# Optimization experiments

Hardware: AMD Instinct MI355X
Metric: run time of the kernel (lower is better)

Reference implementation:

```python
import jax, jax.numpy as jnp
import numpy as np
import math

T, B, D, H, DH, DI, V, L = 1024, 4, 512, 8, 64, 2048, 256, 8
STAGES = (2, 4, 2)   # pre, shortened, post layer counts (model_config)
SF = 4               # fixed boundary every SF tokens
S = T // SF          # number of segments


def setup_inputs() -> dict:
    key = jax.random.key(0)
    ks = jax.random.split(key, 12)
    sd = 0.02
    data = jax.random.randint(ks[0], (T, B), 0, V, dtype=jnp.int32)
    t = jnp.arange(T)
    boundaries_gt = jnp.tile(((t % SF) == (SF - 1)).astype(jnp.int32)[:, None], (1, B))
    return {
        'data': data,
        'boundaries_gt': boundaries_gt,
        'word_emb': jax.random.normal(ks[1], (V, D)) * sd,
        'r_w_bias': jax.random.normal(ks[2], (H, DH)) * sd,
        'r_r_bias': jax.random.normal(ks[3], (H, DH)) * sd,
        'null_group': jax.random.normal(ks[4], (1, 1, D)),
        'down_ln_g': jnp.ones((D,), jnp.float32),
        'down_ln_b': jnp.zeros((D,), jnp.float32),
        'qkv_w': jax.random.normal(ks[5], (L, 3 * H * DH, D)) * sd,
        'rk_w': jax.random.normal(ks[6], (L, H * DH, D)) * sd,
        'o_w': jax.random.normal(ks[7], (L, D, H * DH)) * sd,
        'ln1_g': jnp.ones((L, D), jnp.float32),
        'ln1_b': jnp.zeros((L, D), jnp.float32),
        'ff_w1': jax.random.normal(ks[8], (L, DI, D)) * sd,
        'ff_b1': jnp.zeros((L, DI), jnp.float32),
        'ff_w2': jax.random.normal(ks[9], (L, D, DI)) * sd,
        'ff_b2': jnp.zeros((L, D), jnp.float32),
        'ln2_g': jnp.ones((L, D), jnp.float32),
        'ln2_b': jnp.zeros((L, D), jnp.float32),
        'final_w': jax.random.normal(ks[10], (V, D)) * sd,
        'final_b': jnp.zeros((V,), jnp.float32),
    }


def _ln(x, g, b):
    m = jnp.mean(x, -1, keepdims=True)
    v = jnp.mean((x - m) ** 2, -1, keepdims=True)
    return (x - m) * jax.lax.rsqrt(v + 1e-5) * g + b


def _pos_emb(qlen):
    # sinusoidal relative positions qlen-1 .. 0
    pos = jnp.arange(qlen - 1, -1, -1.0, dtype=jnp.float32)
    inv = 1.0 / (10000.0 ** (jnp.arange(0, D, 2, dtype=jnp.float32) / D))
    ang = pos[:, None] * inv[None, :]
    return jnp.concatenate([jnp.sin(ang), jnp.cos(ang)], -1)  # (qlen, D)


def _rel_shift(x):
    # x: (q, k, b, n) -- Transformer-XL relative shift
    q, k, b, n = x.shape
    x = jnp.pad(x, ((0, 0), (1, 0), (0, 0), (0, 0)))
    return x.reshape(k + 1, q, b, n)[1:].reshape(q, k, b, n)


def _stage(x, P, lo, hi, r_w_bias, r_r_bias):
    qkv_w, rk_w, o_w, ln1_g, ln1_b, w1, b1, w2, b2, ln2_g, ln2_b = P
    qlen, bsz, _ = x.shape
    r = _pos_emb(qlen)
    mask = jnp.triu(jnp.ones((qlen, qlen), bool), 1)  # causal
    scale = 1.0 / math.sqrt(DH)
    for i in range(lo, hi):
        h = x @ qkv_w[i].T                                  # (q,b,3HDh)
        qh, kh, vh = jnp.split(h, 3, axis=-1)
        qh = qh.reshape(qlen, bsz, H, DH)
        kh = kh.reshape(qlen, bsz, H, DH)
        vh = vh.reshape(qlen, bsz, H, DH)
        rk = (r @ rk_w[i].T).reshape(qlen, H, DH)
        AC = jnp.einsum('ibnd,jbnd->ijbn', qh + r_w_bias, kh)
        BD = _rel_shift(jnp.einsum('ibnd,jnd->ijbn', qh + r_r_bias, rk))
        score = jnp.where(mask[:, :, None, None], -1e30, (AC + BD) * scale)
        prob = jax.nn.softmax(score, axis=1)
        vec = jnp.einsum('ijbn,jbnd->ibnd', prob, vh).reshape(qlen, bsz, H * DH)
        x = _ln(x + vec @ o_w[i].T, ln1_g[i], ln1_b[i])      # post-LN
        ff = jax.nn.relu(x @ w1[i].T + b1[i]) @ w2[i].T + b2[i]
        x = _ln(x + ff, ln2_g[i], ln2_b[i])
    return x


def _downsample(bnd, hidden, null_group):
    # bnd: (B,T) float, hidden: (T,B,D). Mean-pool each segment, prepend null group.
    seg = jnp.cumsum(bnd, axis=1) - bnd                      # segment id per token
    ind = (seg[:, :, None] == jnp.arange(S, dtype=bnd.dtype)).astype(hidden.dtype)
    w = ind / (ind.sum(axis=1, keepdims=True) + 1e-9)        # (B,T,S)
    short = jnp.einsum('tbd,bts->sbd', hidden, w)
    null = jnp.tile(null_group, (1, hidden.shape[1], 1))
    return jnp.concatenate([null, short], axis=0)            # (S+1,B,D)


def _upsample(bnd, short):
    # token t copies segment cumsum(bnd)[t] (0 == null group)
    seg = jnp.cumsum(bnd, axis=1).astype(jnp.int32)          # (B,T) in [0,S]
    up = jnp.take_along_axis(short, seg.T[:, :, None], axis=0)  # (T,B,D)
    return up / (1.0 + 1e-9)                                 # matches 1/(1+eps) normalizer


def _forward(data, boundaries_gt, word_emb, r_w_bias, r_r_bias, null_group,
             down_ln_g, down_ln_b, qkv_w, rk_w, o_w, ln1_g, ln1_b,
             ff_w1, ff_b1, ff_w2, ff_b2, ln2_g, ln2_b, final_w, final_b):
    P = (qkv_w, rk_w, o_w, ln1_g, ln1_b, ff_w1, ff_b1, ff_w2, ff_b2, ln2_g, ln2_b)
    hidden = word_emb[data]                                  # (T,B,D)
    hidden = _stage(hidden, P, 0, STAGES[0], r_w_bias, r_r_bias)
    residual = hidden
    hard = boundaries_gt.astype(jnp.float32).T               # (B,T)
    short = _downsample(hard, hidden, null_group)
    short = _ln(short, down_ln_g, down_ln_b)
    short = _stage(short, P, STAGES[0], STAGES[0] + STAGES[1], r_w_bias, r_r_bias)
    hidden = _upsample(hard, short) + residual
    hidden = _stage(hidden, P, STAGES[0] + STAGES[1], L, r_w_bias, r_r_bias)
    return hidden @ final_w.T + final_b                      # logits (T,B,V)


def reference(data, boundaries_gt, word_emb, r_w_bias, r_r_bias, null_group,
              down_ln_g, down_ln_b, qkv_w, rk_w, o_w, ln1_g, ln1_b,
              ff_w1, ff_b1, ff_w2, ff_b2, ln2_g, ln2_b, final_w, final_b):
    return _forward(data, boundaries_gt, word_emb, r_w_bias, r_r_bias, null_group,
                    down_ln_g, down_ln_b, qkv_w, rk_w, o_w, ln1_g, ln1_b,
                    ff_w1, ff_b1, ff_w2, ff_b2, ln2_g, ln2_b, final_w, final_b)
```

## Files before the change

### kernel.cpp

```cpp
#include <hip/hip_runtime.h>
#include <math.h>

#define T_  1024
#define B_  4
#define D_  512
#define H_  8
#define DH_ 64
#define DI_ 2048
#define V_  256
#define L_  8
#define S_  256

typedef _Float16 f16;
typedef f16   f16x8 __attribute__((ext_vector_type(8)));
typedef float f32x4 __attribute__((ext_vector_type(4)));

__device__ __forceinline__ void gload16(const void* g, void* l) {
    __builtin_amdgcn_global_load_lds(
        (const __attribute__((address_space(1))) void*)g,
        (__attribute__((address_space(3))) void*)l, 16, 0, 0);
}

__constant__ int cIT[24] = {15,15,14,13,12,11,10, 9,  8, 7,14, 6,13, 5,12, 4,  8, 0, 9, 1,10, 2,11, 3};
__constant__ int cT0[24] = { 0, 8, 0, 0, 0, 0, 0, 0,  0, 0, 8, 0, 8, 0, 8, 0,  8, 0, 8, 0, 8, 0, 8, 0};
__constant__ int cT1[24] = { 8,16, 8, 8, 8, 8, 8, 8,  8, 8,15, 7,14, 6,13, 5,  9, 1,10, 2,11, 3,12, 4};
__constant__ int cIT2[8] = {4,4,3,3,2,2,1,0};
__constant__ int cT02[8] = {0,3,0,2,0,2,0,0};
__constant__ int cT12[8] = {3,5,2,4,2,3,2,1};

__global__ __launch_bounds__(256) void k_f2h(const float* __restrict__ s,
                                             f16* __restrict__ d, int n) {
    int i = (blockIdx.x * 256 + threadIdx.x) * 4;
    int stride = gridDim.x * 1024;
    for (; i < n; i += stride) {
        float4 v = *(const float4*)(s + i);
        d[i + 0] = (f16)v.x; d[i + 1] = (f16)v.y;
        d[i + 2] = (f16)v.z; d[i + 3] = (f16)v.w;
    }
}

__global__ __launch_bounds__(256) void k_embed(const int* __restrict__ data,
                                               const float* __restrict__ emb,
                                               float* __restrict__ x,
                                               f16* __restrict__ xh) {
    int idx = blockIdx.x * 256 + threadIdx.x;
    if (idx >= T_ * B_ * D_) return;
    int d  = idx & (D_ - 1);
    int tb = idx >> 9;
    float v = emb[(size_t)data[tb] * D_ + d];
    x[idx] = v; xh[idx] = (f16)v;
}

__global__ __launch_bounds__(256) void k_posemb(f16* __restrict__ r, int qlen) {
    int p = blockIdx.x;
    int k = threadIdx.x;
    float pos = (float)(qlen - 1 - p);
    float inv = powf(10000.f, -((float)k) / 256.f);
    float ang = pos * inv;
    r[(size_t)p * D_ + k]       = (f16)sinf(ang);
    r[(size_t)p * D_ + 256 + k] = (f16)cosf(ang);
}

template<int BM, int BN, int OUT16, int ACT>
__global__ __launch_bounds__(256) void k_gemm(const f16* __restrict__ X, int lda,
                                              const f16* __restrict__ W,
                                              const float* __restrict__ bias,
                                              void* __restrict__ Yv,
                                              int M, int N, int K) {
    __shared__ f16 As[BM * 64];
    __shared__ f16 Bs[BN * 64];
    const int tid = threadIdx.x, w = tid >> 6, lane = tid & 63;
    const int l16 = lane & 15, lg = lane >> 4;
    int nwg = gridDim.x * gridDim.y;
    int bid = blockIdx.y * gridDim.x + blockIdx.x;
    if ((nwg & 7) == 0) bid = (bid & 7) * (nwg >> 3) + (bid >> 3);
    const int bm = (bid % gridDim.x) * BM, bn = (bid / gridDim.x) * BN;
    const int lrow = lane >> 3, lcol = (lane & 7) * 8;
    constexpr int AI = (BM >= 32) ? BM / 32 : 1;
    constexpr int BI = BN / 32;
    constexpr int MI = (BN == 128) ? 4 : BM / 32;
    constexpr int NJ = 2;
    const int rbase = (BN == 128) ? 0 : (w >> 1) * (BM / 2);
    const int cbase = (BN == 128) ? w * 32 : (w & 1) * 32;
    const f32x4 z4 = {0.f, 0.f, 0.f, 0.f};
    f32x4 acc[MI][NJ];
    #pragma unroll
    for (int i = 0; i < MI; ++i)
        #pragma unroll
        for (int j = 0; j < NJ; ++j) acc[i][j] = z4;

    for (int k0 = 0; k0 < K; k0 += 64) {
        __syncthreads();
        #pragma unroll
        for (int u = 0; u < AI; ++u) {
            int rb = w * (BM / 4) + u * 8;
            gload16(X + (size_t)(bm + rb + lrow) * lda + k0 + lcol, &As[rb * 64]);
        }
        #pragma unroll
        for (int u = 0; u < BI; ++u) {
            int rb = w * (BN / 4) + u * 8;
            gload16(W + (size_t)(bn + rb + lrow) * K + k0 + lcol, &Bs[rb * 64]);
        }
        __syncthreads();
        __builtin_amdgcn_s_setprio(1);
        #pragma unroll
        for (int h = 0; h < 2; ++h) {
            f16x8 af[MI], bf[NJ];
            #pragma unroll
            for (int i = 0; i < MI; ++i)
                af[i] = *(const f16x8*)&As[(rbase + i * 16 + l16) * 64 + h * 32 + lg * 8];
            #pragma unroll
            for (int j = 0; j < NJ; ++j)
                bf[j] = *(const f16x8*)&Bs[(cbase + j * 16 + l16) * 64 + h * 32 + lg * 8];
            #pragma unroll
            for (int i = 0; i < MI; ++i)
                #pragma unroll
                for (int j = 0; j < NJ; ++j)
                    acc[i][j] = __builtin_amdgcn_mfma_f32_16x16x32_f16(af[i], bf[j], acc[i][j], 0, 0, 0);
        }
        __builtin_amdgcn_s_setprio(0);
    }
    #pragma unroll
    for (int i = 0; i < MI; ++i) {
        #pragma unroll
        for (int r = 0; r < 4; ++r) {
            int row = bm + rbase + i * 16 + lg * 4 + r;
            if (row >= M) continue;
            int colb = bn + cbase + l16;
            #pragma unroll
            for (int j = 0; j < NJ; ++j) {
                float v = acc[i][j][r];
                if (bias) v += bias[colb + j * 16];
                if (ACT) v = fmaxf(v, 0.f);
                if (OUT16) ((f16*)Yv)[(size_t)row * N + colb + j * 16] = (f16)v;
                else       ((float*)Yv)[(size_t)row * N + colb + j * 16] = v;
            }
        }
    }
}

__global__ __launch_bounds__(256) void k_ln(float* __restrict__ x,
                                            const f16* __restrict__ add,
                                            const float* __restrict__ g,
                                            const float* __restrict__ b,
                                            f16* __restrict__ xh, int rows) {
    int row = blockIdx.x * 4 + (threadIdx.x >> 6);
    if (row >= rows) return;
    int lane = threadIdx.x & 63;
    float* xr = x + (size_t)row * D_ + lane * 8;
    float v[8];
    {
        float4 a0 = *(const float4*)xr;
        float4 a1 = *(const float4*)(xr + 4);
        v[0] = a0.x; v[1] = a0.y; v[2] = a0.z; v[3] = a0.w;
        v[4] = a1.x; v[5] = a1.y; v[6] = a1.z; v[7] = a1.w;
    }
    if (add) {
        f16x8 a = *(const f16x8*)(add + (size_t)row * D_ + lane * 8);
        #pragma unroll
        for (int u = 0; u < 8; ++u) v[u] += (float)a[u];
    }
    float s = 0.f, sq = 0.f;
    #pragma unroll
    for (int u = 0; u < 8; ++u) { s += v[u]; sq += v[u] * v[u]; }
    #pragma unroll
    for (int off = 1; off < 64; off <<= 1) {
        s  += __shfl_xor(s,  off, 64);
        sq += __shfl_xor(sq, off, 64);
    }
    float mean = s * (1.f / (float)D_);
    float var  = sq * (1.f / (float)D_) - mean * mean;
    float rs   = rsqrtf(var + 1e-5f);
    const float* gp = g + lane * 8;
    const float* bp = b + lane * 8;
    float4 g0 = *(const float4*)gp, g1 = *(const float4*)(gp + 4);
    float4 b0 = *(const float4*)bp, b1 = *(const float4*)(bp + 4);
    float gg[8] = {g0.x, g0.y, g0.z, g0.w, g1.x, g1.y, g1.z, g1.w};
    float bb[8] = {b0.x, b0.y, b0.z, b0.w, b1.x, b1.y, b1.z, b1.w};
    float o[8];
    #pragma unroll
    for (int u = 0; u < 8; ++u) o[u] = (v[u] - mean) * rs * gg[u] + bb[u];
    *(float4*)xr       = make_float4(o[0], o[1], o[2], o[3]);
    *(float4*)(xr + 4) = make_float4(o[4], o[5], o[6], o[7]);
    f16x8 hv;
    #pragma unroll
    for (int u = 0; u < 8; ++u) hv[u] = (f16)o[u];
    *(f16x8*)(xh + (size_t)row * D_ + lane * 8) = hv;
}

__global__ __launch_bounds__(256) void k_downln(const float* __restrict__ x,
                                                const float* __restrict__ nullg,
                                                const float* __restrict__ g,
                                                const float* __restrict__ bi,
                                                float* __restrict__ xs,
                                                f16* __restrict__ xsh) {
    int row = blockIdx.x * 4 + (threadIdx.x >> 6);
    if (row >= (S_ + 1) * B_) return;
    int lane = threadIdx.x & 63;
    int s = row >> 2, b = row & 3;
    float v[8];
    if (s == 0) {
        const float* np = nullg + lane * 8;
        float4 a0 = *(const float4*)np, a1 = *(const float4*)(np + 4);
        v[0] = a0.x; v[1] = a0.y; v[2] = a0.z; v[3] = a0.w;
        v[4] = a1.x; v[5] = a1.y; v[6] = a1.z; v[7] = a1.w;
    } else {
        int t0 = (s - 1) * 4;
        #pragma unroll
        for (int u = 0; u < 8; ++u) v[u] = 0.f;
        #pragma unroll
        for (int k = 0; k < 4; ++k) {
            const float* xp = x + ((size_t)(t0 + k) * B_ + b) * D_ + lane * 8;
            float4 a0 = *(const float4*)xp, a1 = *(const float4*)(xp + 4);
            v[0] += a0.x; v[1] += a0.y; v[2] += a0.z; v[3] += a0.w;
            v[4] += a1.x; v[5] += a1.y; v[6] += a1.z; v[7] += a1.w;
        }
        #pragma unroll
        for (int u = 0; u < 8; ++u) v[u] *= 0.25f;
    }
    float sm = 0.f, sq = 0.f;
    #pragma unroll
    for (int u = 0; u < 8; ++u) { sm += v[u]; sq += v[u] * v[u]; }
    #pragma unroll
    for (int off = 1; off < 64; off <<= 1) {
        sm += __shfl_xor(sm, off, 64);
        sq += __shfl_xor(sq, off, 64);
    }
    float mean = sm * (1.f / (float)D_);
    float var  = sq * (1.f / (float)D_) - mean * mean;
    float rs   = rsqrtf(var + 1e-5f);
    float o[8];
    #pragma unroll
    for (int u = 0; u < 8; ++u)
        o[u] = (v[u] - mean) * rs * g[lane * 8 + u] + bi[lane * 8 + u];
    float* xp = xs + (size_t)row * D_ + lane * 8;
    *(float4*)xp       = make_float4(o[0], o[1], o[2], o[3]);
    *(float4*)(xp + 4) = make_float4(o[4], o[5], o[6], o[7]);
    f16x8 hv;
    #pragma unroll
    for (int u = 0; u < 8; ++u) hv[u] = (f16)o[u];
    *(f16x8*)(xsh + (size_t)row * D_ + lane * 8) = hv;
}

__global__ __launch_bounds__(256) void k_up(float* __restrict__ x,
                                            const float* __restrict__ xs,
                                            f16* __restrict__ xh) {
    int idx = blockIdx.x * 256 + threadIdx.x;
    if (idx >= T_ * B_ * D_) return;
    int d  = idx & (D_ - 1);
    int tb = idx >> 9;
    int t = tb >> 2, b = tb & 3;
    int seg = (t + 1) >> 2;
    float v = x[idx] + xs[((size_t)seg * B_ + b) * D_ + d];
    x[idx] = v; xh[idx] = (f16)v;
}

__global__ __launch_bounds__(256) void k_attn(f16* __restrict__ qkv,
                                              const f16* __restrict__ rkb,
                                              int ldr,
                                              const float* __restrict__ rwb,
                                              const float* __restrict__ rrb,
                                              int Q, float* __restrict__ part) {
    __shared__ f16 RKs[192 * 64];
    __shared__ f16 Ks[64 * 64];
    __shared__ f16 Vt[64 * 72];
    __shared__ f16 Pl[4][16 * 72];
    f16* Qw = RKs;
    f16* Qr = RKs + 4096;

    int it, t0, t1, b, n;
    bool partial;
    int idxp;
    {
        int p = blockIdx.y * gridDim.x + blockIdx.x;
        int xcd = p & 7, qq = p >> 3;
        b = xcd >> 1;
        n = (xcd & 1) * 4 + (qq & 3);
        int slot = qq >> 2;
        if (Q == 1024) {
            it = cIT[slot]; t0 = cT0[slot]; t1 = cT1[slot];
            partial = (it >= 8);
            idxp = (b * 8 + n) * 8 + (it - 8);
        } else {
            it = cIT2[slot]; t0 = cT02[slot]; t1 = cT12[slot];
            partial = (it >= 2);
            idxp = (b * 8 + n) * 3 + (it - 2);
        }
    }
    const int i0 = it * 64;
    const int tid = threadIdx.x, w = tid >> 6, lane = tid & 63;
    const int l16 = lane & 15, lg = lane >> 4;
    const int xsw = (l16 & 7) << 3;
    const int gr8 = lane >> 3;
    const int gsl = ((lane & 7) ^ gr8) * 8;
    const int vjj = tid >> 2, vdb = (tid & 3) * 16;
    const int wb = 48 - w * 16;
    const f32x4 z4 = {0.f, 0.f, 0.f, 0.f};

    {
        int row = tid >> 2, dq = (tid & 3) * 16;
        const f16* qp = qkv + ((size_t)(i0 + row) * B_ + b) * 1536 + n * 64 + dq;
        f16x8 q0 = *(const f16x8*)qp, q1 = *(const f16x8*)(qp + 8);
        int rsw = (row & 7) << 3;
        #pragma unroll
        for (int u = 0; u < 8; ++u) {
            float qa = (float)q0[u], qb2 = (float)q1[u];
            Qw[row * 64 + ((dq + u) ^ rsw)]     = (f16)(qa + rwb[n * 64 + dq + u]);
            Qw[row * 64 + ((dq + 8 + u) ^ rsw)] = (f16)(qb2 + rwb[n * 64 + dq + 8 + u]);
            Qr[row * 64 + ((dq + u) ^ rsw)]     = (f16)(qa + rrb[n * 64 + dq + u]);
            Qr[row * 64 + ((dq + 8 + u) ^ rsw)] = (f16)(qb2 + rrb[n * 64 + dq + 8 + u]);
        }
    }
    __syncthreads();
    f16x8 aqw[2], aqr[2];
    #pragma unroll
    for (int h = 0; h < 2; ++h) {
        aqw[h] = *(const f16x8*)&Qw[(w * 16 + l16) * 64 + ((h * 32 + lg * 8) ^ xsw)];
        aqr[h] = *(const f16x8*)&Qr[(w * 16 + l16) * 64 + ((h * 32 + lg * 8) ^ xsw)];
    }
    __syncthreads();

    const long long pb = (long long)Q - 64 - i0;
    #pragma unroll
    for (int u = 0; u < 4; ++u) {
        int rb = w * 32 + u * 8;
        long long p = pb + t0 * 64 + rb + gr8;
        gload16(rkb + p * ldr + n * 64 + gsl, &RKs[rb * 64]);
    }
    #pragma unroll
    for (int u = 0; u < 2; ++u) {
        int rb = w * 16 + u * 8;
        gload16(qkv + ((size_t)(t0 * 64 + rb + gr8) * B_ + b) * 1536 + 512 + n * 64 + gsl,
                &Ks[rb * 64]);
    }
    f16x8 vr0, vr1;
    {
        const f16* vp = qkv + ((size_t)(t0 * 64 + vjj) * B_ + b) * 1536 + 1024 + n * 64 + vdb;
        vr0 = *(const f16x8*)vp; vr1 = *(const f16x8*)(vp + 8);
    }

    f32x4 acc[4]; acc[0] = z4; acc[1] = z4; acc[2] = z4; acc[3] = z4;
    float psum[4] = {0.f, 0.f, 0.f, 0.f};
    int base = 0;

    for (int t = t0; t < t1; ++t) {
        const int j0 = t * 64;
        __syncthreads();
        #pragma unroll
        for (int u = 0; u < 8; ++u) {
            Vt[(vdb + u) * 72 + (vjj ^ ((u & 7) << 3))]     = vr0[u];
            Vt[(vdb + 8 + u) * 72 + (vjj ^ ((u & 7) << 3))] = vr1[u];
        }
        if (t + 1 < t1) {
            int sb = base + 128; if (sb >= 192) sb -= 192;
            #pragma unroll
            for (int u = 0; u < 2; ++u) {
                int rb = w * 16 + u * 8;
                long long p = pb + j0 + 128 + rb + gr8;
                gload16(rkb + p * ldr + n * 64 + gsl, &RKs[(sb + rb) * 64]);
            }
        }
        f32x4 s1[4]; s1[0] = z4; s1[1] = z4; s1[2] = z4; s1[3] = z4;
        __builtin_amdgcn_s_setprio(1);
        #pragma unroll
        for (int f = 0; f < 4; ++f)
            #pragma unroll
            for (int h = 0; h < 2; ++h) {
                f16x8 bv = *(const f16x8*)&Ks[(f * 16 + l16) * 64 + ((h * 32 + lg * 8) ^ xsw)];
                s1[f] = __builtin_amdgcn_mfma_f32_16x16x32_f16(aqw[h], bv, s1[f], 0, 0, 0);
            }
        __builtin_amdgcn_s_setprio(0);
        if (t + 1 < t1) {
            const f16* vp = qkv + ((size_t)(j0 + 64 + vjj) * B_ + b) * 1536 + 1024 + n * 64 + vdb;
            vr0 = *(const f16x8*)vp; vr1 = *(const f16x8*)(vp + 8);
        }
        f32x4 s2[5]; s2[0] = z4; s2[1] = z4; s2[2] = z4; s2[3] = z4; s2[4] = z4;
        __builtin_amdgcn_s_setprio(1);
        #pragma unroll
        for (int f = 0; f < 5; ++f) {
            int slot = base + wb + f * 16 + l16; if (slot >= 192) slot -= 192;
            #pragma unroll
            for (int h = 0; h < 2; ++h) {
                f16x8 bv = *(const f16x8*)&RKs[slot * 64 + ((h * 32 + lg * 8) ^ xsw)];
                s2[f] = __builtin_amdgcn_mfma_f32_16x16x32_f16(aqr[h], bv, s2[f], 0, 0, 0);
            }
        }
        __builtin_amdgcn_s_setprio(0);
        #pragma unroll
        for (int r = 0; r < 4; ++r) {
            const int q = lg * 4 + r;
            const int iq = i0 + w * 16 + q;
            const int src = (lane & 48) | ((l16 + 15 - q) & 15);
            float g0 = __shfl(s2[0][r], src, 64);
            float g1 = __shfl(s2[1][r], src, 64);
            float g2 = __shfl(s2[2][r], src, 64);
            float g3 = __shfl(s2[3][r], src, 64);
            float g4 = __shfl(s2[4][r], src, 64);
            const bool hi = l16 > q;
            float sv[4];
            sv[0] = (s1[0][r] + (hi ? g1 : g0)) * 0.125f;
            sv[1] = (s1[1][r] + (hi ? g2 : g1)) * 0.125f;
            sv[2] = (s1[2][r] + (hi ? g3 : g2)) * 0.125f;
            sv[3] = (s1[3][r] + (hi ? g4 : g3)) * 0.125f;
            #pragma unroll
            for (int h = 0; h < 4; ++h) {
                int j = j0 + h * 16 + l16;
                if (j > iq || j >= Q) sv[h] = -1e30f;
            }
            float p0 = __expf(sv[0]), p1 = __expf(sv[1]);
            float p2 = __expf(sv[2]), p3 = __expf(sv[3]);
            psum[r] += (p0 + p1) + (p2 + p3);
            Pl[w][q * 72 + l16]      = (f16)p0;
            Pl[w][q * 72 + 16 + l16] = (f16)p1;
            Pl[w][q * 72 + 32 + l16] = (f16)p2;
            Pl[w][q * 72 + 48 + l16] = (f16)p3;
        }
        __syncthreads();
        f16x8 pa0 = *(const f16x8*)&Pl[w][l16 * 72 + lg * 8];
        f16x8 pa1 = *(const f16x8*)&Pl[w][l16 * 72 + 32 + lg * 8];
        __builtin_amdgcn_s_setprio(1);
        #pragma unroll
        for (int f = 0; f < 4; ++f) {
            f16x8 bv0 = *(const f16x8*)&Vt[(f * 16 + l16) * 72 + ((lg * 8) ^ xsw)];
            acc[f] = __builtin_amdgcn_mfma_f32_16x16x32_f16(pa0, bv0, acc[f], 0, 0, 0);
            f16x8 bv1 = *(const f16x8*)&Vt[(f * 16 + l16) * 72 + ((32 + lg * 8) ^ xsw)];
            acc[f] = __builtin_amdgcn_mfma_f32_16x16x32_f16(pa1, bv1, acc[f], 0, 0, 0);
        }
        __builtin_amdgcn_s_setprio(0);
        if (t + 1 < t1) {
            #pragma unroll
            for (int u = 0; u < 2; ++u) {
                int rb = w * 16 + u * 8;
                gload16(qkv + ((size_t)(j0 + 64 + rb + gr8) * B_ + b) * 1536 + 512 + n * 64 + gsl,
                        &Ks[rb * 64]);
            }
        }
        base += 64; if (base >= 192) base -= 192;
    }
    if (partial) {
        float* Pp = part + (size_t)idxp * 8320 + (t0 ? 4160 : 0);
        #pragma unroll
        for (int r = 0; r < 4; ++r) {
            float ps = psum[r];
            ps += __shfl_xor(ps, 1, 64);
            ps += __shfl_xor(ps, 2, 64);
            ps += __shfl_xor(ps, 4, 64);
            ps += __shfl_xor(ps, 8, 64);
            int row = w * 16 + lg * 4 + r;
            #pragma unroll
            for (int f = 0; f < 4; ++f)
                Pp[row * 64 + f * 16 + l16] = acc[f][r];
            if (l16 == 0) Pp[4096 + row] = ps;
        }
    } else {
        #pragma unroll
        for (int r = 0; r < 4; ++r) {
            float ps = psum[r];
            ps += __shfl_xor(ps, 1, 64);
            ps += __shfl_xor(ps, 2, 64);
            ps += __shfl_xor(ps, 4, 64);
            ps += __shfl_xor(ps, 8, 64);
            int i = i0 + w * 16 + lg * 4 + r;
            if (i < Q) {
                float inv = 1.f / ps;
                f16* op = qkv + ((size_t)i * B_ + b) * 1536 + n * 64;
                #pragma unroll
                for (int f = 0; f < 4; ++f)
                    op[f * 16 + l16] = (f16)(acc[f][r] * inv);
            }
        }
    }
}

__global__ __launch_bounds__(256) void k_comb(const float* __restrict__ part,
                                              f16* __restrict__ qkv,
                                              int nm, int itbase, int Q) {
    int idxp = blockIdx.x;
    int m = idxp % nm;
    int bn = idxp / nm;
    int b = bn >> 3, n = bn & 7;
    int i0 = (m + itbase) * 64;
    int row = threadIdx.x >> 2, dp = (threadIdx.x & 3) * 16;
    if (i0 + row >= Q) return;
    const float* A  = part + (size_t)idxp * 8320;
    const float* Bp = A + 4160;
    float inv = 1.f / (A[4096 + row] + Bp[4096 + row]);
    f16* op = qkv + ((size_t)(i0 + row) * B_ + b) * 1536 + n * 64 + dp;
    #pragma unroll
    for (int k = 0; k < 16; k += 4) {
        float4 a  = *(const float4*)(A  + row * 64 + dp + k);
        float4 bb = *(const float4*)(Bp + row * 64 + dp + k);
        op[k + 0] = (f16)((a.x + bb.x) * inv);
        op[k + 1] = (f16)((a.y + bb.y) * inv);
        op[k + 2] = (f16)((a.z + bb.z) * inv);
        op[k + 3] = (f16)((a.w + bb.w) * inv);
    }
}

extern "C" void kernel_launch(void* const* d_in, const int* in_sizes, int n_in,
                              void* d_out, int out_size, void* d_ws, size_t ws_size,
                              hipStream_t stream) {
    const int*   data     = (const int*)  d_in[0];
    const float* word_emb = (const float*)d_in[2];
    const float* rwb      = (const float*)d_in[3];
    const float* rrb      = (const float*)d_in[4];
    const float* nullg    = (const float*)d_in[5];
    const float* dg       = (const float*)d_in[6];
    const float* db       = (const float*)d_in[7];
    const float* qkv_w    = (const float*)d_in[8];
    const float* rk_w     = (const float*)d_in[9];
    const float* o_w      = (const float*)d_in[10];
    const float* ln1g     = (const float*)d_in[11];
    const float* ln1b     = (const float*)d_in[12];
    const float* w1       = (const float*)d_in[13];
    const float* b1       = (const float*)d_in[14];
    const float* w2       = (const float*)d_in[15];
    const float* b2       = (const float*)d_in[16];
    const float* ln2g     = (const float*)d_in[17];
    const float* ln2b     = (const float*)d_in[18];
    const float* fw       = (const float*)d_in[19];
    const float* fb       = (const float*)d_in[20];
    float* out = (float*)d_out;
    float* ws  = (float*)d_ws;

    float* x    = ws;
    float* tmp  = x + 2097152;
    float* xs   = tmp + 2097152;
    f16* xh     = (f16*)(xs + 589824);
    f16* xsh    = xh + 2097152;
    f16* r1h    = xsh + 589824;
    f16* r2h    = r1h + 524288;
    f16* rkall  = r2h + 163840;
    f16* bigh   = rkall + 2623488;
    f16* qkv_wh = bigh + 8388608;
    f16* rk_wh  = qkv_wh + 6291456;
    f16* o_wh   = rk_wh + 2097152;
    f16* w1h    = o_wh + 2097152;
    f16* w2h    = w1h + 8388608;
    f16* fwh    = w2h + 8388608;
    f16* tmph   = (f16*)tmp;

    auto conv = [&](const float* s, f16* d, int n) {
        int blocks = min(2048, (n + 1023) / 1024);
        k_f2h<<<blocks, 256, 0, stream>>>(s, d, n);
    };
    conv(qkv_w, qkv_wh, L_ * 1536 * 512);
    conv(rk_w,  rk_wh,  L_ * 512 * 512);
    conv(o_w,   o_wh,   L_ * 512 * 512);
    conv(w1,    w1h,    L_ * 2048 * 512);
    conv(w2,    w2h,    L_ * 512 * 2048);
    conv(fw,    fwh,    256 * 512);

    auto gemm = [&](const f16* Xp, int lda, const f16* Wp, const float* bp,
                    void* Yp, int M, int N, int K, int out16, int act) {
        int b64_128 = (N % 128 == 0) ? ((M + 63) / 64) * (N / 128) : 0;
        if (b64_128 >= 768) {
            dim3 g((M + 63) / 64, N / 128);
            if (out16) {
                if (act) k_gemm<64, 128, 1, 1><<<g, 256, 0, stream>>>(Xp, lda, Wp, bp, Yp, M, N, K);
                else     k_gemm<64, 128, 1, 0><<<g, 256, 0, stream>>>(Xp, lda, Wp, bp, Yp, M, N, K);
            } else      k_gemm<64, 128, 0, 0><<<g, 256, 0, stream>>>(Xp, lda, Wp, bp, Yp, M, N, K);
            return;
        }
        int b64_64 = ((M + 63) / 64) * (N / 64);
        if (b64_64 >= 768) {
            dim3 g((M + 63) / 64, N / 64);
            if (out16) {
                if (act) k_gemm<64, 64, 1, 1><<<g, 256, 0, stream>>>(Xp, lda, Wp, bp, Yp, M, N, K);
                else     k_gemm<64, 64, 1, 0><<<g, 256, 0, stream>>>(Xp, lda, Wp, bp, Yp, M, N, K);
            } else      k_gemm<64, 64, 0, 0><<<g, 256, 0, stream>>>(Xp, lda, Wp, bp, Yp, M, N, K);
            return;
        }
        dim3 g((M + 31) / 32, N / 64);
        if (out16) {
            if (act) k_gemm<32, 64, 1, 1><<<g, 256, 0, stream>>>(Xp, lda, Wp, bp, Yp, M, N, K);
            else     k_gemm<32, 64, 1, 0><<<g, 256, 0, stream>>>(Xp, lda, Wp, bp, Yp, M, N, K);
        } else      k_gemm<32, 64, 0, 0><<<g, 256, 0, stream>>>(Xp, lda, Wp, bp, Yp, M, N, K);
    };

    k_embed<<<8192, 256, 0, stream>>>(data, word_emb, x, xh);
    k_posemb<<<1024, 256, 0, stream>>>(r1h, 1024);
    k_posemb<<<257, 256, 0, stream>>>(r2h, 257);

    gemm(r1h, 512, rk_wh,                nullptr, rkall,           1024, 1024, 512, 1, 0);
    gemm(r1h, 512, rk_wh + 6 * 262144,   nullptr, rkall + 1048576, 1024, 1024, 512, 1, 0);
    gemm(r2h, 512, rk_wh + 2 * 262144,   nullptr, rkall + 2097152,  257, 2048, 512, 1, 0);

    auto stage = [&](float* xb, f16* xbh, int Q, int lo, int hi) {
        const int M = Q * B_;
        dim3 gA = (Q == 1024) ? dim3(24, 32) : dim3(8, 32);
        dim3 gL((M + 3) / 4);
        for (int i = lo; i < hi; ++i) {
            const f16* rkp; int ldr;
            if (i < 2)       { rkp = rkall + i * 512;                 ldr = 1024; }
            else if (i >= 6) { rkp = rkall + 1048576 + (i - 6) * 512; ldr = 1024; }
            else             { rkp = rkall + 2097152 + (i - 2) * 512; ldr = 2048; }
            gemm(xbh, 512, qkv_wh + (size_t)i * 786432, nullptr, bigh, M, 1536, 512, 1, 0);
            k_attn<<<gA, 256, 0, stream>>>(bigh, rkp, ldr, rwb, rrb, Q, tmp);
            if (Q == 1024) k_comb<<<256, 256, 0, stream>>>(tmp, bigh, 8, 8, 1024);
            else           k_comb<<<96, 256, 0, stream>>>(tmp, bigh, 3, 2, 257);
            gemm(bigh, 1536, o_wh + (size_t)i * 262144, nullptr, tmph, M, 512, 512, 1, 0);
            k_ln<<<gL, 256, 0, stream>>>(xb, tmph, ln1g + (size_t)i * 512, ln1b + (size_t)i * 512, xbh, M);
            gemm(xbh, 512, w1h + (size_t)i * 1048576, b1 + (size_t)i * 2048, bigh, M, 2048, 512, 1, 1);
            gemm(bigh, 2048, w2h + (size_t)i * 1048576, b2 + (size_t)i * 512, tmph, M, 512, 2048, 1, 0);
            k_ln<<<gL, 256, 0, stream>>>(xb, tmph, ln2g + (size_t)i * 512, ln2b + (size_t)i * 512, xbh, M);
        }
    };

    stage(x, xh, 1024, 0, 2);
    k_downln<<<257, 256, 0, stream>>>(x, nullg, dg, db, xs, xsh);
    stage(xs, xsh, S_ + 1, 2, 6);
    k_up<<<8192, 256, 0, stream>>>(x, xs, xh);
    stage(x, xh, 1024, 6, 8);
    gemm(xh, 512, fwh, fb, out, T_ * B_, V_, 512, 0, 0);
}
```

Baseline: 851.9 us.

## Drop fp32 residual stream, add split-K for short stage, merge weight conversion

Removes the fp32 residual copy and keeps the hidden state only in fp16, so layernorm, downsample and upsample read and write half the bytes. Adds split-K for the out-projection and FFN2 GEMMs in the shortened stage, with the partial sums reduced inside the layernorm kernel. Also merges the six weight-conversion launches into one, vectorises the embed and upsample kernels, and replaces powf with exp2f. Keeping the residual in fp16 loses precision across layers, and writing partials out to memory adds traffic.

Result: faster. 778.3 us (-8.6%).

```diff
diff --git a/kernel.cpp b/kernel.cpp
--- a/kernel.cpp
+++ b/kernel.cpp
@@ -13,6 +13,7 @@
 
 typedef _Float16 f16;
 typedef f16   f16x8 __attribute__((ext_vector_type(8)));
+typedef f16   f16x4 __attribute__((ext_vector_type(4)));
 typedef float f32x4 __attribute__((ext_vector_type(4)));
 
 __device__ __forceinline__ void gload16(const void* g, void* l) {
@@ -28,34 +29,42 @@
 __constant__ int cT02[8] = {0,3,0,2,0,2,0,0};
 __constant__ int cT12[8] = {3,5,2,4,2,3,2,1};
 
-__global__ __launch_bounds__(256) void k_f2h(const float* __restrict__ s,
-                                             f16* __restrict__ d, int n) {
-    int i = (blockIdx.x * 256 + threadIdx.x) * 4;
+__global__ __launch_bounds__(256) void k_f2hall(
+        const float* s0, f16* d0, int n0, const float* s1, f16* d1, int n1,
+        const float* s2, f16* d2, int n2, const float* s3, f16* d3, int n3,
+        const float* s4, f16* d4, int n4, const float* s5, f16* d5, int n5) {
+    int start = (blockIdx.x * 256 + threadIdx.x) * 4;
     int stride = gridDim.x * 1024;
-    for (; i < n; i += stride) {
-        float4 v = *(const float4*)(s + i);
-        d[i + 0] = (f16)v.x; d[i + 1] = (f16)v.y;
-        d[i + 2] = (f16)v.z; d[i + 3] = (f16)v.w;
+    const float* ss[6] = {s0, s1, s2, s3, s4, s5};
+    f16* dd[6] = {d0, d1, d2, d3, d4, d5};
+    int nn[6] = {n0, n1, n2, n3, n4, n5};
+    for (int seg = 0; seg < 6; ++seg) {
+        const float* s = ss[seg]; f16* d = dd[seg]; int n = nn[seg];
+        for (int i = start; i < n; i += stride) {
+            float4 v = *(const float4*)(s + i);
+            f16x4 h = {(f16)v.x, (f16)v.y, (f16)v.z, (f16)v.w};
+            *(f16x4*)(d + i) = h;
+        }
     }
 }
 
 __global__ __launch_bounds__(256) void k_embed(const int* __restrict__ data,
                                                const float* __restrict__ emb,
-                                               float* __restrict__ x,
                                                f16* __restrict__ xh) {
-    int idx = blockIdx.x * 256 + threadIdx.x;
-    if (idx >= T_ * B_ * D_) return;
-    int d  = idx & (D_ - 1);
-    int tb = idx >> 9;
-    float v = emb[(size_t)data[tb] * D_ + d];
-    x[idx] = v; xh[idx] = (f16)v;
+    int i4 = (blockIdx.x * 256 + threadIdx.x) * 4;
+    if (i4 >= T_ * B_ * D_) return;
+    int d  = i4 & (D_ - 1);
+    int tb = i4 >> 9;
+    float4 v = *(const float4*)(emb + (size_t)data[tb] * D_ + d);
+    f16x4 h = {(f16)v.x, (f16)v.y, (f16)v.z, (f16)v.w};
+    *(f16x4*)(xh + i4) = h;
 }
 
 __global__ __launch_bounds__(256) void k_posemb(f16* __restrict__ r, int qlen) {
     int p = blockIdx.x;
     int k = threadIdx.x;
     float pos = (float)(qlen - 1 - p);
-    float inv = powf(10000.f, -((float)k) / 256.f);
+    float inv = exp2f((float)k * -0.05190512648f);
     float ang = pos * inv;
     r[(size_t)p * D_ + k]       = (f16)sinf(ang);
     r[(size_t)p * D_ + 256 + k] = (f16)cosf(ang);
@@ -75,8 +84,11 @@
     int bid = blockIdx.y * gridDim.x + blockIdx.x;
     if ((nwg & 7) == 0) bid = (bid & 7) * (nwg >> 3) + (bid >> 3);
     const int bm = (bid % gridDim.x) * BM, bn = (bid / gridDim.x) * BN;
+    const int Kz = K / gridDim.z;
+    const int kbeg = blockIdx.z * Kz, kend = kbeg + Kz;
+    const size_t zofs = (size_t)blockIdx.z * M * N;
     const int lrow = lane >> 3, lcol = (lane & 7) * 8;
-    constexpr int AI = (BM >= 32) ? BM / 32 : 1;
+    constexpr int AI = BM / 32;
     constexpr int BI = BN / 32;
     constexpr int MI = (BN == 128) ? 4 : BM / 32;
     constexpr int NJ = 2;
@@ -89,7 +101,7 @@
         #pragma unroll
         for (int j = 0; j < NJ; ++j) acc[i][j] = z4;
 
-    for (int k0 = 0; k0 < K; k0 += 64) {
+    for (int k0 = kbeg; k0 < kend; k0 += 64) {
         __syncthreads();
         #pragma unroll
         for (int u = 0; u < AI; ++u) {
@@ -120,6 +132,7 @@
         }
         __builtin_amdgcn_s_setprio(0);
     }
+    const bool dob = bias && (blockIdx.z == 0);
     #pragma unroll
     for (int i = 0; i < MI; ++i) {
         #pragma unroll
@@ -130,45 +143,46 @@
             #pragma unroll
             for (int j = 0; j < NJ; ++j) {
                 float v = acc[i][j][r];
-                if (bias) v += bias[colb + j * 16];
+                if (dob) v += bias[colb + j * 16];
                 if (ACT) v = fmaxf(v, 0.f);
-                if (OUT16) ((f16*)Yv)[(size_t)row * N + colb + j * 16] = (f16)v;
+                if (OUT16) ((f16*)Yv)[zofs + (size_t)row * N + colb + j * 16] = (f16)v;
                 else       ((float*)Yv)[(size_t)row * N + colb + j * 16] = v;
             }
         }
     }
 }
 
-__global__ __launch_bounds__(256) void k_ln(float* __restrict__ x,
+__global__ __launch_bounds__(256) void k_ln(f16* __restrict__ xh,
                                             const f16* __restrict__ add,
+                                            int nadd, int astr,
                                             const float* __restrict__ g,
                                             const float* __restrict__ b,
-                                            f16* __restrict__ xh, int rows) {
+                                            int rows) {
     int row = blockIdx.x * 4 + (threadIdx.x >> 6);
     if (row >= rows) return;
     int lane = threadIdx.x & 63;
-    float* xr = x + (size_t)row * D_ + lane * 8;
+    f16* xr = xh + (size_t)row * D_ + lane * 8;
     float v[8];
     {
-        float4 a0 = *(const float4*)xr;
-        float4 a1 = *(const float4*)(xr + 4);
-        v[0] = a0.x; v[1] = a0.y; v[2] = a0.z; v[3] = a0.w;
-        v[4] = a1.x; v[5] = a1.y; v[6] = a1.z; v[7] = a1.w;
-    }
-    if (add) {
-        f16x8 a = *(const f16x8*)(add + (size_t)row * D_ + lane * 8);
+        f16x8 a = *(const f16x8*)xr;
+        #pragma unroll
+        for (int u = 0; u < 8; ++u) v[u] = (float)a[u];
+    }
+    const f16* ap = add + (size_t)row * D_ + lane * 8;
+    for (int s = 0; s < nadd; ++s) {
+        f16x8 a = *(const f16x8*)(ap + (size_t)s * astr);
         #pragma unroll
         for (int u = 0; u < 8; ++u) v[u] += (float)a[u];
     }
-    float s = 0.f, sq = 0.f;
-    #pragma unroll
-    for (int u = 0; u < 8; ++u) { s += v[u]; sq += v[u] * v[u]; }
+    float sm = 0.f, sq = 0.f;
+    #pragma unroll
+    for (int u = 0; u < 8; ++u) { sm += v[u]; sq += v[u] * v[u]; }
     #pragma unroll
     for (int off = 1; off < 64; off <<= 1) {
-        s  += __shfl_xor(s,  off, 64);
+        sm += __shfl_xor(sm, off, 64);
         sq += __shfl_xor(sq, off, 64);
     }
-    float mean = s * (1.f / (float)D_);
+    float mean = sm * (1.f / (float)D_);
     float var  = sq * (1.f / (float)D_) - mean * mean;
     float rs   = rsqrtf(var + 1e-5f);
     const float* gp = g + lane * 8;
@@ -177,22 +191,16 @@
     float4 b0 = *(const float4*)bp, b1 = *(const float4*)(bp + 4);
     float gg[8] = {g0.x, g0.y, g0.z, g0.w, g1.x, g1.y, g1.z, g1.w};
     float bb[8] = {b0.x, b0.y, b0.z, b0.w, b1.x, b1.y, b1.z, b1.w};
-    float o[8];
-    #pragma unroll
-    for (int u = 0; u < 8; ++u) o[u] = (v[u] - mean) * rs * gg[u] + bb[u];
-    *(float4*)xr       = make_float4(o[0], o[1], o[2], o[3]);
-    *(float4*)(xr + 4) = make_float4(o[4], o[5], o[6], o[7]);
     f16x8 hv;
     #pragma unroll
-    for (int u = 0; u < 8; ++u) hv[u] = (f16)o[u];
-    *(f16x8*)(xh + (size_t)row * D_ + lane * 8) = hv;
-}
-
-__global__ __launch_bounds__(256) void k_downln(const float* __restrict__ x,
+    for (int u = 0; u < 8; ++u) hv[u] = (f16)((v[u] - mean) * rs * gg[u] + bb[u]);
+    *(f16x8*)xr = hv;
+}
+
+__global__ __launch_bounds__(256) void k_downln(const f16* __restrict__ xh,
                                                 const float* __restrict__ nullg,
                                                 const float* __restrict__ g,
                                                 const float* __restrict__ bi,
-                                                float* __restrict__ xs,
                                                 f16* __restrict__ xsh) {
     int row = blockIdx.x * 4 + (threadIdx.x >> 6);
     if (row >= (S_ + 1) * B_) return;
@@ -210,10 +218,9 @@
         for (int u = 0; u < 8; ++u) v[u] = 0.f;
         #pragma unroll
         for (int k = 0; k < 4; ++k) {
-            const float* xp = x + ((size_t)(t0 + k) * B_ + b) * D_ + lane * 8;
-            float4 a0 = *(const float4*)xp, a1 = *(const float4*)(xp + 4);
-            v[0] += a0.x; v[1] += a0.y; v[2] += a0.z; v[3] += a0.w;
-            v[4] += a1.x; v[5] += a1.y; v[6] += a1.z; v[7] += a1.w;
+            f16x8 a = *(const f16x8*)(xh + ((size_t)(t0 + k) * B_ + b) * D_ + lane * 8);
+            #pragma unroll
+            for (int u = 0; u < 8; ++u) v[u] += (float)a[u];
         }
         #pragma unroll
         for (int u = 0; u < 8; ++u) v[u] *= 0.25f;
@@ -229,30 +236,27 @@
     float mean = sm * (1.f / (float)D_);
     float var  = sq * (1.f / (float)D_) - mean * mean;
     float rs   = rsqrtf(var + 1e-5f);
-    float o[8];
+    f16x8 hv;
     #pragma unroll
     for (int u = 0; u < 8; ++u)
-        o[u] = (v[u] - mean) * rs * g[lane * 8 + u] + bi[lane * 8 + u];
-    float* xp = xs + (size_t)row * D_ + lane * 8;
-    *(float4*)xp       = make_float4(o[0], o[1], o[2], o[3]);
-    *(float4*)(xp + 4) = make_float4(o[4], o[5], o[6], o[7]);
-    f16x8 hv;
-    #pragma unroll
-    for (int u = 0; u < 8; ++u) hv[u] = (f16)o[u];
+        hv[u] = (f16)((v[u] - mean) * rs * g[lane * 8 + u] + bi[lane * 8 + u]);
     *(f16x8*)(xsh + (size_t)row * D_ + lane * 8) = hv;
 }
 
-__global__ __launch_bounds__(256) void k_up(float* __restrict__ x,
-                                            const float* __restrict__ xs,
-                                            f16* __restrict__ xh) {
-    int idx = blockIdx.x * 256 + threadIdx.x;
-    if (idx >= T_ * B_ * D_) return;
-    int d  = idx & (D_ - 1);
-    int tb = idx >> 9;
+__global__ __launch_bounds__(256) void k_up(f16* __restrict__ xh,
+                                            const f16* __restrict__ xsh) {
+    int i8 = (blockIdx.x * 256 + threadIdx.x) * 8;
+    if (i8 >= T_ * B_ * D_) return;
+    int d  = i8 & (D_ - 1);
+    int tb = i8 >> 9;
     int t = tb >> 2, b = tb & 3;
     int seg = (t + 1) >> 2;
-    float v = x[idx] + xs[((size_t)seg * B_ + b) * D_ + d];
-    x[idx] = v; xh[idx] = (f16)v;
+    f16x8 a = *(const f16x8*)(xh + i8);
+    f16x8 u2 = *(const f16x8*)(xsh + ((size_t)seg * B_ + b) * D_ + d);
+    f16x8 o;
+    #pragma unroll
+    for (int u = 0; u < 8; ++u) o[u] = (f16)((float)a[u] + (float)u2[u]);
+    *(f16x8*)(xh + i8) = o;
 }
 
 __global__ __launch_bounds__(256) void k_attn(f16* __restrict__ qkv,
@@ -523,10 +527,9 @@
     float* out = (float*)d_out;
     float* ws  = (float*)d_ws;
 
-    float* x    = ws;
-    float* tmp  = x + 2097152;
-    float* xs   = tmp + 2097152;
-    f16* xh     = (f16*)(xs + 589824);
+    float* ov   = ws;
+    f16* tmph   = (f16*)ov;
+    f16* xh     = (f16*)(ov + 2129920);
     f16* xsh    = xh + 2097152;
     f16* r1h    = xsh + 589824;
     f16* r2h    = r1h + 524288;
@@ -538,21 +541,22 @@
     f16* w1h    = o_wh + 2097152;
     f16* w2h    = w1h + 8388608;
     f16* fwh    = w2h + 8388608;
-    f16* tmph   = (f16*)tmp;
-
-    auto conv = [&](const float* s, f16* d, int n) {
-        int blocks = min(2048, (n + 1023) / 1024);
-        k_f2h<<<blocks, 256, 0, stream>>>(s, d, n);
-    };
-    conv(qkv_w, qkv_wh, L_ * 1536 * 512);
-    conv(rk_w,  rk_wh,  L_ * 512 * 512);
-    conv(o_w,   o_wh,   L_ * 512 * 512);
-    conv(w1,    w1h,    L_ * 2048 * 512);
-    conv(w2,    w2h,    L_ * 512 * 2048);
-    conv(fw,    fwh,    256 * 512);
+
+    k_f2hall<<<2048, 256, 0, stream>>>(
+        qkv_w, qkv_wh, L_ * 1536 * 512,
+        rk_w,  rk_wh,  L_ * 512 * 512,
+        o_w,   o_wh,   L_ * 512 * 512,
+        w1,    w1h,    L_ * 2048 * 512,
+        w2,    w2h,    L_ * 512 * 2048,
+        fw,    fwh,    256 * 512);
 
     auto gemm = [&](const f16* Xp, int lda, const f16* Wp, const float* bp,
-                    void* Yp, int M, int N, int K, int out16, int act) {
+                    void* Yp, int M, int N, int K, int out16, int act, int splitk) {
+        if (splitk > 1) {
+            dim3 g((M + 31) / 32, N / 64, splitk);
+            k_gemm<32, 64, 1, 0><<<g, 256, 0, stream>>>(Xp, lda, Wp, bp, Yp, M, N, K);
+            return;
+        }
         int b64_128 = (N % 128 == 0) ? ((M + 63) / 64) * (N / 128) : 0;
         if (b64_128 >= 768) {
             dim3 g((M + 63) / 64, N / 128);
@@ -578,39 +582,43 @@
         } else      k_gemm<32, 64, 0, 0><<<g, 256, 0, stream>>>(Xp, lda, Wp, bp, Yp, M, N, K);
     };
 
-    k_embed<<<8192, 256, 0, stream>>>(data, word_emb, x, xh);
+    k_embed<<<2048, 256, 0, stream>>>(data, word_emb, xh);
     k_posemb<<<1024, 256, 0, stream>>>(r1h, 1024);
     k_posemb<<<257, 256, 0, stream>>>(r2h, 257);
 
-    gemm(r1h, 512, rk_wh,                nullptr, rkall,           1024, 1024, 512, 1, 0);
-    gemm(r1h, 512, rk_wh + 6 * 262144,   nullptr, rkall + 1048576, 1024, 1024, 512, 1, 0);
-    gemm(r2h, 512, rk_wh + 2 * 262144,   nullptr, rkall + 2097152,  257, 2048, 512, 1, 0);
-
-    auto stage = [&](float* xb, f16* xbh, int Q, int lo, int hi) {
+    gemm(r1h, 512, rk_wh,              nullptr, rkall,           1024, 1024, 512, 1, 0, 1);
+    gemm(r1h, 512, rk_wh + 6 * 262144, nullptr, rkall + 1048576, 1024, 1024, 512, 1, 0, 1);
+    gemm(r2h, 512, rk_wh + 2 * 262144, nullptr, rkall + 2097152,  257, 2048, 512, 1, 0, 1);
+
+    auto stage = [&](f16* xbh, int Q, int lo, int hi) {
         const int M = Q * B_;
         dim3 gA = (Q == 1024) ? dim3(24, 32) : dim3(8, 32);
         dim3 gL((M + 3) / 4);
+        const int sk_o  = (Q == 1024) ? 1 : 2;
+        const int sk_w2 = (Q == 1024) ? 1 : 4;
         for (int i = lo; i < hi; ++i) {
             const f16* rkp; int ldr;
             if (i < 2)       { rkp = rkall + i * 512;                 ldr = 1024; }
             else if (i >= 6) { rkp = rkall + 1048576 + (i - 6) * 512; ldr = 1024; }
             else             { rkp = rkall + 2097152 + (i - 2) * 512; ldr = 2048; }
-            gemm(xbh, 512, qkv_wh + (size_t)i * 786432, nullptr, bigh, M, 1536, 512, 1, 0);
-            k_attn<<<gA, 256, 0, stream>>>(bigh, rkp, ldr, rwb, rrb, Q, tmp);
-            if (Q == 1024) k_comb<<<256, 256, 0, stream>>>(tmp, bigh, 8, 8, 1024);
-            else           k_comb<<<96, 256, 0, stream>>>(tmp, bigh, 3, 2, 257);
-            gemm(bigh, 1536, o_wh + (size_t)i * 262144, nullptr, tmph, M, 512, 512, 1, 0);
-            k_ln<<<gL, 256, 0, stream>>>(xb, tmph, ln1g + (size_t)i * 512, ln1b + (size_t)i * 512, xbh, M);
-            gemm(xbh, 512, w1h + (size_t)i * 1048576, b1 + (size_t)i * 2048, bigh, M, 2048, 512, 1, 1);
-            gemm(bigh, 2048, w2h + (size_t)i * 1048576, b2 + (size_t)i * 512, tmph, M, 512, 2048, 1, 0);
-            k_ln<<<gL, 256, 0, stream>>>(xb, tmph, ln2g + (size_t)i * 512, ln2b + (size_t)i * 512, xbh, M);
+            gemm(xbh, 512, qkv_wh + (size_t)i * 786432, nullptr, bigh, M, 1536, 512, 1, 0, 1);
+            k_attn<<<gA, 256, 0, stream>>>(bigh, rkp, ldr, rwb, rrb, Q, ov);
+            if (Q == 1024) k_comb<<<256, 256, 0, stream>>>(ov, bigh, 8, 8, 1024);
+            else           k_comb<<<96, 256, 0, stream>>>(ov, bigh, 3, 2, 257);
+            gemm(bigh, 1536, o_wh + (size_t)i * 262144, nullptr, tmph, M, 512, 512, 1, 0, sk_o);
+            k_ln<<<gL, 256, 0, stream>>>(xbh, tmph, sk_o, M * 512,
+                                         ln1g + (size_t)i * 512, ln1b + (size_t)i * 512, M);
+            gemm(xbh, 512, w1h + (size_t)i * 1048576, b1 + (size_t)i * 2048, bigh, M, 2048, 512, 1, 1, 1);
+            gemm(bigh, 2048, w2h + (size_t)i * 1048576, b2 + (size_t)i * 512, tmph, M, 512, 2048, 1, 0, sk_w2);
+            k_ln<<<gL, 256, 0, stream>>>(xbh, tmph, sk_w2, M * 512,
+                                         ln2g + (size_t)i * 512, ln2b + (size_t)i * 512, M);
         }
     };
 
-    stage(x, xh, 1024, 0, 2);
-    k_downln<<<257, 256, 0, stream>>>(x, nullg, dg, db, xs, xsh);
-    stage(xs, xsh, S_ + 1, 2, 6);
-    k_up<<<8192, 256, 0, stream>>>(x, xs, xh);
-    stage(x, xh, 1024, 6, 8);
-    gemm(xh, 512, fwh, fb, out, T_ * B_, V_, 512, 0, 0);
-}
+    stage(xh, 1024, 0, 2);
+    k_downln<<<257, 256, 0, stream>>>(xh, nullg, dg, db, xsh);
+    stage(xsh, S_ + 1, 2, 6);
+    k_up<<<1024, 256, 0, stream>>>(xh, xsh);
+    stage(xh, 1024, 6, 8);
+    gemm(xh, 512, fwh, fb, out, T_ * B_, V_, 512, 0, 0, 1);
+}
```
